# Performance work log

Hardware: AMD Instinct MI355X
Metric: run time of the kernel (lower is better)

## Reference

```python
import jax, jax.numpy as jnp
import numpy as np

STAGE = 100  # number of weight bins


def _bin_reconstruct(w, affine):
    # Faithful vectorization of the 100-iter binning loop: element in bin i
    # (half-open interval) gets scaled by affine[i]; the max element falls
    # outside every bin (w < wmin + stage*range/stage fails) and is zeroed.
    flat = w.reshape(-1)
    wmin, wmax = flat.min(), flat.max()
    idx = jnp.floor((flat - wmin) / (wmax - wmin) * STAGE).astype(jnp.int32)
    mask = (idx < STAGE).astype(flat.dtype)  # mask is detached in torch (non-diff anyway)
    scale = affine[jnp.clip(idx, 0, STAGE - 1)]
    return flat * scale * mask


def _kl_vs_laplace(new_flat, lap):
    # F.kl_div(log_softmax(w), softmax(lap), reduction='none').mean()
    logq = jax.nn.log_softmax(new_flat)
    p = jax.nn.softmax(lap)
    return (p * (jnp.log(p) - logq)).mean()


def _adder2d(x, w, stride, padding, groups=1):
    # AdderNet conv: out = -sum_k |patch_k - w_k| (no bias)
    O, Cg, kh, kw = w.shape
    patches = jax.lax.conv_general_dilated_patches(
        x, (kh, kw), (stride, stride), [(padding, padding), (padding, padding)])
    B, _, Hp, Wp = patches.shape  # channel dim ordered (C, kh, kw), C-major
    if groups == 1:
        p = patches.reshape(B, 1, Cg * kh * kw, Hp, Wp)
        wf = w.reshape(1, O, Cg * kh * kw, 1, 1)
    else:  # depthwise: groups == C_in, Cg == 1, O == C_in
        p = patches.reshape(B, O, kh * kw, Hp, Wp)
        wf = w.reshape(1, O, kh * kw, 1, 1)
    return -jnp.abs(p - wf).sum(axis=2)  # [B, O, Hp, Wp]


def _bn_train(x, g, b, eps=1e-5):
    # BatchNorm2d in training mode (batch statistics, biased variance)
    m = x.mean(axis=(0, 2, 3), keepdims=True)
    v = ((x - m) ** 2).mean(axis=(0, 2, 3), keepdims=True)
    return (x - m) * jax.lax.rsqrt(v + eps) * g.reshape(1, -1, 1, 1) + b.reshape(1, -1, 1, 1)


def _forward(x, sw_ds, sw_c1, sw_c2, sw_c3, a_ds, a_c1, a_c2, a_c3, peg_w,
             g1, b1, g2, b2, g3, b3, gds, bds, lap_ds, lap_c1, lap_c2, lap_c3):
    kl = jnp.float32(0.0)
    f_ds = _bin_reconstruct(sw_ds, a_ds)
    kl = kl + _kl_vs_laplace(f_ds, lap_ds)
    f_c1 = _bin_reconstruct(sw_c1, a_c1)
    kl = kl + _kl_vs_laplace(f_c1, lap_c1)
    residual = jax.nn.relu(_bn_train(_adder2d(x, f_ds.reshape(sw_ds.shape), 1, 0), gds, bds))
    h = _adder2d(x, f_c1.reshape(sw_c1.shape), 1, 0)
    h = _adder2d(h, peg_w, 1, 1, groups=peg_w.shape[0])  # PEG depthwise 3x3
    h = jax.nn.relu(_bn_train(h, g1, b1))
    f_c2 = _bin_reconstruct(sw_c2, a_c2)
    kl = kl + _kl_vs_laplace(f_c2, lap_c2)
    h = _adder2d(h, f_c2.reshape(sw_c2.shape), 1, 1)
    h = jax.nn.relu(_bn_train(h, g2, b2))
    f_c3 = _bin_reconstruct(sw_c3, a_c3)
    kl = kl + _kl_vs_laplace(f_c3, lap_c3)
    h = _adder2d(h, f_c3.reshape(sw_c3.shape), 1, 0)
    h = _bn_train(h, g3, b3)  # bn3 gamma zero-initialized
    return jax.nn.relu(h + residual), kl


def setup_inputs() -> dict:
    key = jax.random.key(0)
    ks = jax.random.split(key, 16)
    inp = {
        'x': jax.random.normal(ks[0], (4, 128, 28, 28), jnp.float32),
        'sw_downsample': jax.random.normal(ks[1], (256, 128, 1, 1), jnp.float32) * 0.05,
        'sw_conv1': jax.random.normal(ks[2], (64, 128, 1, 1), jnp.float32) * 0.05,
        'sw_conv2': jax.random.normal(ks[3], (64, 64, 3, 3), jnp.float32) * 0.05,
        'sw_conv3': jax.random.normal(ks[4], (256, 64, 1, 1), jnp.float32) * 0.05,
        'downsample_affine': jax.random.normal(ks[5], (100,), jnp.float32),
        'conv1_affine': jax.random.normal(ks[6], (100,), jnp.float32),
        'conv2_affine': jax.random.normal(ks[7], (100,), jnp.float32),
        'conv3_affine': jax.random.normal(ks[8], (100,), jnp.float32),
        'peg_w': jax.random.normal(ks[9], (64, 1, 3, 3), jnp.float32) * 0.05,
        'bn1_g': jnp.ones((64,), jnp.float32), 'bn1_b': jnp.zeros((64,), jnp.float32),
        'bn2_g': jnp.ones((64,), jnp.float32), 'bn2_b': jnp.zeros((64,), jnp.float32),
        'bn3_g': jnp.zeros((256,), jnp.float32), 'bn3_b': jnp.zeros((256,), jnp.float32),
        'bnds_g': jnp.ones((256,), jnp.float32), 'bnds_b': jnp.zeros((256,), jnp.float32),
        # Laplace(0, 2) samples, drawn once in setup so the reference is deterministic
        'lap_ds': jax.random.laplace(ks[10], (32768,), jnp.float32) * 2.0,
        'lap_c1': jax.random.laplace(ks[11], (8192,), jnp.float32) * 2.0,
        'lap_c2': jax.random.laplace(ks[12], (36864,), jnp.float32) * 2.0,
        'lap_c3': jax.random.laplace(ks[13], (16384,), jnp.float32) * 2.0,
    }
    return inp


def reference(x, sw_downsample, sw_conv1, sw_conv2, sw_conv3,
              downsample_affine, conv1_affine, conv2_affine, conv3_affine, peg_w,
              bn1_g, bn1_b, bn2_g, bn2_b, bn3_g, bn3_b, bnds_g, bnds_b,
              lap_ds, lap_c1, lap_c2, lap_c3):
    return _forward(x, sw_downsample, sw_conv1, sw_conv2, sw_conv3,
                    downsample_affine, conv1_affine, conv2_affine, conv3_affine, peg_w,
                    bn1_g, bn1_b, bn2_g, bn2_b, bn3_g, bn3_b, bnds_g, bnds_b,
                    lap_ds, lap_c1, lap_c2, lap_c3)
```

## Files before the change

kernel.cpp:

```cpp
#include <hip/hip_runtime.h>
#include <math.h>


#define HW 784
#define NB 4
#define STAGE 100

__device__ __forceinline__ float wredSum(float v){
  for (int o = 32; o > 0; o >>= 1) v += __shfl_down(v, o, 64);
  return v;
}
__device__ __forceinline__ float wredMax(float v){
  for (int o = 32; o > 0; o >>= 1) v = fmaxf(v, __shfl_down(v, o, 64));
  return v;
}
__device__ __forceinline__ float wredMin(float v){
  for (int o = 32; o > 0; o >>= 1) v = fminf(v, __shfl_down(v, o, 64));
  return v;
}
__device__ __forceinline__ double wredSumD(double v){
  for (int o = 32; o > 0; o >>= 1) v += __shfl_down(v, o, 64);
  return v;
}

__device__ float blockMin4(float v){
  __shared__ float shn[4];
  __syncthreads();
  v = wredMin(v);
  if ((threadIdx.x & 63) == 0) shn[threadIdx.x >> 6] = v;
  __syncthreads();
  return fminf(fminf(shn[0], shn[1]), fminf(shn[2], shn[3]));
}
__device__ float blockMax4(float v){
  __shared__ float shx[4];
  __syncthreads();
  v = wredMax(v);
  if ((threadIdx.x & 63) == 0) shx[threadIdx.x >> 6] = v;
  __syncthreads();
  return fmaxf(fmaxf(shx[0], shx[1]), fmaxf(shx[2], shx[3]));
}

__device__ void stats4(float v0, float v1, float v2, float v3,
                       double* sumP, double* sqP, int oc0){
  __shared__ double sred[4][8];
  __syncthreads();
  const int w = threadIdx.x >> 6;
  float vv[4] = {v0, v1, v2, v3};
  #pragma unroll
  for (int i = 0; i < 4; i++){
    double d = (double)vv[i];
    double s = wredSumD(d);
    double q = wredSumD(d * d);
    if ((threadIdx.x & 63) == 0){ sred[w][i] = s; sred[w][4 + i] = q; }
  }
  __syncthreads();
  if (threadIdx.x < 8){
    double tot = sred[0][threadIdx.x] + sred[1][threadIdx.x]
               + sred[2][threadIdx.x] + sred[3][threadIdx.x];
    int i = threadIdx.x & 3;
    if (threadIdx.x < 4) atomicAdd(&sumP[oc0 + i], tot);
    else                 atomicAdd(&sqP[oc0 + i],  tot);
  }
}
__device__ void stats2(float v0, float v1, double* sumP, double* sqP, int oc0){
  __shared__ double sred2[4][4];
  __syncthreads();
  const int w = threadIdx.x >> 6;
  float vv[2] = {v0, v1};
  #pragma unroll
  for (int i = 0; i < 2; i++){
    double d = (double)vv[i];
    double s = wredSumD(d);
    double q = wredSumD(d * d);
    if ((threadIdx.x & 63) == 0){ sred2[w][i] = s; sred2[w][2 + i] = q; }
  }
  __syncthreads();
  if (threadIdx.x < 4){
    double tot = sred2[0][threadIdx.x] + sred2[1][threadIdx.x]
               + sred2[2][threadIdx.x] + sred2[3][threadIdx.x];
    int i = threadIdx.x & 1;
    if (threadIdx.x < 2) atomicAdd(&sumP[oc0 + i], tot);
    else                 atomicAdd(&sqP[oc0 + i],  tot);
  }
}

__device__ void klAccum(float se, float sel, float sef, float sq, double* dst){
  __shared__ double kls[4][4];
  __syncthreads();
  const int w = threadIdx.x >> 6;
  double a0 = wredSumD((double)se);
  double a1 = wredSumD((double)sel);
  double a2 = wredSumD((double)sef);
  double a3 = wredSumD((double)sq);
  if ((threadIdx.x & 63) == 0){
    kls[w][0] = a0; kls[w][1] = a1; kls[w][2] = a2; kls[w][3] = a3;
  }
  __syncthreads();
  if (threadIdx.x < 4){
    double tot = kls[0][threadIdx.x] + kls[1][threadIdx.x]
               + kls[2][threadIdx.x] + kls[3][threadIdx.x];
    atomicAdd(&dst[threadIdx.x], tot);
  }
}

__device__ __forceinline__ float reconv(float vv, float mn, float rng,
                                        const float* saff){
  float q = (vv - mn) / rng * 100.0f;
  int idx = (int)floorf(q);
  float nv = 0.0f;
  if (idx < STAGE){
    int ci = idx < 0 ? 0 : (idx > STAGE - 1 ? STAGE - 1 : idx);
    nv = vv * saff[ci];
  }
  return nv;
}

__device__ __forceinline__ void mmReduce(const float* mmbuf, int tens,
                                         float& mn, float& mx){
  mn = 3.402823466e38f; mx = -3.402823466e38f;
  #pragma unroll
  for (int k = 0; k < 16; k++){
    mn = fminf(mn, mmbuf[tens * 32 + k]);
    mx = fmaxf(mx, mmbuf[tens * 32 + 16 + k]);
  }
}

__global__ __launch_bounds__(256) void minmax_kernel(
    const float* w0, int n0, const float* w1, int n1,
    const float* w2, int n2, const float* w3, int n3,
    float* mmbuf, double* dstat)
{
  if (threadIdx.x < 21) dstat[blockIdx.x * 21 + threadIdx.x] = 0.0;
  const int tens = blockIdx.x >> 4, slot = blockIdx.x & 15;
  const float* w; int n;
  if      (tens == 0){ w = w0; n = n0; }
  else if (tens == 1){ w = w1; n = n1; }
  else if (tens == 2){ w = w2; n = n2; }
  else               { w = w3; n = n3; }
  float mn = 3.402823466e38f, mx = -3.402823466e38f;
  for (int i = slot * 256 + threadIdx.x; i < n; i += 4096){
    float v = w[i];
    mn = fminf(mn, v); mx = fmaxf(mx, v);
  }
  mn = blockMin4(mn); mx = blockMax4(mx);
  if (threadIdx.x == 0){
    mmbuf[tens * 32 + slot]      = mn;
    mmbuf[tens * 32 + 16 + slot] = mx;
  }
}

__global__ __launch_bounds__(256) void front_kernel(
    const float* __restrict__ x,
    const float* __restrict__ w_ds, const float* __restrict__ aff_ds,
    const float* __restrict__ lap_ds,
    const float* __restrict__ w_c1, const float* __restrict__ aff_c1,
    const float* __restrict__ lap_c1,
    const float* __restrict__ w_c2, const float* __restrict__ aff_c2,
    const float* __restrict__ lap_c2, float* __restrict__ f_c2,
    const float* __restrict__ w_c3, const float* __restrict__ aff_c3,
    const float* __restrict__ lap_c3,
    const float* __restrict__ peg_w, const float* __restrict__ mmbuf,
    float* __restrict__ A, float* __restrict__ T2, double* __restrict__ dS)
{
  const int t = threadIdx.x;
  if (blockIdx.x < 512){
    const int a = blockIdx.x;
    const int chunk = a & 3, og = (a >> 2) & 31, b = a >> 7;
    const int oc0 = og * 8;
    __shared__ float saff[STAGE];
    __shared__ float sw[1024];
    if (t < STAGE) saff[t] = aff_ds[t];
    float mn, mx; mmReduce(mmbuf, 0, mn, mx);
    const float rng = mx - mn;
    __syncthreads();
    for (int k = t; k < 1024; k += 256)
      sw[k] = reconv(w_ds[oc0 * 128 + k], mn, rng, saff);
    __syncthreads();

    const int px = chunk * 196 + t;
    float v0=0,v1=0,v2=0,v3=0,v4=0,v5=0,v6=0,v7=0;
    if (t < 196){
      const float* xp = x + (size_t)b * 128 * HW + px;
      float c0=0,c1=0,c2=0,c3=0,c4=0,c5=0,c6=0,c7=0;
      #pragma unroll 4
      for (int c = 0; c < 128; c++){
        float xv = xp[(size_t)c * HW];
        c0 += fabsf(xv - sw[c]);
        c1 += fabsf(xv - sw[128 + c]);
        c2 += fabsf(xv - sw[256 + c]);
        c3 += fabsf(xv - sw[384 + c]);
        c4 += fabsf(xv - sw[512 + c]);
        c5 += fabsf(xv - sw[640 + c]);
        c6 += fabsf(xv - sw[768 + c]);
        c7 += fabsf(xv - sw[896 + c]);
      }
      v0=-c0; v1=-c1; v2=-c2; v3=-c3; v4=-c4; v5=-c5; v6=-c6; v7=-c7;
      float* op = A + ((size_t)(b * 256 + oc0)) * HW + px;
      op[0]=v0; op[HW]=v1; op[2*HW]=v2; op[3*HW]=v3;
      op[4*HW]=v4; op[5*HW]=v5; op[6*HW]=v6; op[7*HW]=v7;
    }
    stats4(v0, v1, v2, v3, dS + 0, dS + 256, oc0);
    stats4(v4, v5, v6, v7, dS + 0, dS + 256, oc0 + 4);

    if (b == 0 && chunk == 0){
      float se = 0, sel = 0, sef = 0, sq = 0;
      for (int k = t; k < 1024; k += 256){
        float l = lap_ds[oc0 * 128 + k];
        float e = expf(l);
        se += e; sel += e * l; sef += e * sw[k];
        sq += expf(sw[k]);
      }
      klAccum(se, sel, sef, sq, dS + 1280 + 0);
    }
  } else if (blockIdx.x < 768){
    const int a = blockIdx.x - 512;
    const int rc = a & 3, og = (a >> 2) & 15, b = a >> 6;
    const int oc0 = og * 4;
    __shared__ float saffc[STAGE];
    __shared__ float swc[512];
    __shared__ float swp[36];
    __shared__ float sT1[4][256];
    if (t < STAGE) saffc[t] = aff_c1[t];
    if (t >= 128 && t < 164) swp[t - 128] = peg_w[oc0 * 9 + (t - 128)];
    float mn, mx; mmReduce(mmbuf, 1, mn, mx);
    const float rng = mx - mn;
    __syncthreads();
    for (int k = t; k < 512; k += 256)
      swc[k] = reconv(w_c1[oc0 * 128 + k], mn, rng, saffc);
    __syncthreads();

    if (t < 252){
      const int rr = t / 28;
      const int col = t - rr * 28;
      const int wr = rc * 7 - 1 + rr;
      float tv0 = 0, tv1 = 0, tv2 = 0, tv3 = 0;
      if (wr >= 0 && wr < 28){
        const float* xp = x + (size_t)b * 128 * HW + wr * 28 + col;
        float c0 = 0, c1 = 0, c2 = 0, c3 = 0;
        #pragma unroll 4
        for (int c = 0; c < 128; c++){
          float xv = xp[(size_t)c * HW];
          c0 += fabsf(xv - swc[c]);
          c1 += fabsf(xv - swc[128 + c]);
          c2 += fabsf(xv - swc[256 + c]);
          c3 += fabsf(xv - swc[384 + c]);
        }
        tv0 = -c0; tv1 = -c1; tv2 = -c2; tv3 = -c3;
      }
      sT1[0][t] = tv0; sT1[1][t] = tv1; sT1[2][t] = tv2; sT1[3][t] = tv3;
    }
    __syncthreads();
    float v0 = 0, v1 = 0, v2 = 0, v3 = 0;
    if (t < 196){
      const int r = t / 28, col = t - r * 28;
      float c0 = 0, c1 = 0, c2 = 0, c3 = 0;
      #pragma unroll
      for (int ky = 0; ky < 3; ky++){
        #pragma unroll
        for (int kx = 0; kx < 3; kx++){
          int cc = col + kx - 1;
          bool ok = (cc >= 0) && (cc < 28);
          int idx = ok ? ((r + ky) * 28 + cc) : 0;
          float p0 = ok ? sT1[0][idx] : 0.0f;
          float p1 = ok ? sT1[1][idx] : 0.0f;
          float p2 = ok ? sT1[2][idx] : 0.0f;
          float p3 = ok ? sT1[3][idx] : 0.0f;
          int wk = ky * 3 + kx;
          c0 += fabsf(p0 - swp[wk]);
          c1 += fabsf(p1 - swp[9 + wk]);
          c2 += fabsf(p2 - swp[18 + wk]);
          c3 += fabsf(p3 - swp[27 + wk]);
        }
      }
      v0 = -c0; v1 = -c1; v2 = -c2; v3 = -c3;
      const int opx = (rc * 7 + r) * 28 + col;
      float* op = T2 + ((size_t)(b * 64 + oc0)) * HW + opx;
      op[0] = v0; op[HW] = v1; op[2 * HW] = v2; op[3 * HW] = v3;
    }
    stats4(v0, v1, v2, v3, dS + 512, dS + 576, oc0);

    if (b == 0 && rc == 0){
      float se = 0, sel = 0, sef = 0, sq = 0;
      for (int k = t; k < 512; k += 256){
        float l = lap_c1[oc0 * 128 + k];
        float e = expf(l);
        se += e; sel += e * l; sef += e * swc[k];
        sq += expf(swc[k]);
      }
      klAccum(se, sel, sef, sq, dS + 1280 + 4);
    }
  } else if (blockIdx.x < 832){
    const int j = blockIdx.x - 768;
    __shared__ float saff2[STAGE];
    if (t < STAGE) saff2[t] = aff_c2[t];
    float mn, mx; mmReduce(mmbuf, 2, mn, mx);
    const float rng = mx - mn;
    __syncthreads();
    float se = 0, sel = 0, sef = 0, sq = 0;
    for (int k = t; k < 576; k += 256){
      float nv = reconv(w_c2[j * 576 + k], mn, rng, saff2);
      f_c2[j * 576 + k] = nv;
      float l = lap_c2[j * 576 + k];
      float e = expf(l);
      se += e; sel += e * l; sef += e * nv; sq += expf(nv);
    }
    klAccum(se, sel, sef, sq, dS + 1280 + 8);
  } else {
    const int j = blockIdx.x - 832;
    __shared__ float saff3[STAGE];
    if (t < STAGE) saff3[t] = aff_c3[t];
    float mn, mx; mmReduce(mmbuf, 3, mn, mx);
    const float rng = mx - mn;
    __syncthreads();
    float se = 0, sel = 0, sef = 0, sq = 0;
    for (int k = t; k < 1024; k += 256){
      float nv = reconv(w_c3[j * 1024 + k], mn, rng, saff3);
      float l = lap_c3[j * 1024 + k];
      float e = expf(l);
      se += e; sel += e * l; sef += e * nv; sq += expf(nv);
    }
    klAccum(se, sel, sef, sq, dS + 1280 + 12);
  }
}

__global__ __launch_bounds__(256) void bnapply_pad_kernel(
    const float* __restrict__ T2, float* __restrict__ T2b,
    const float* __restrict__ g1, const float* __restrict__ b1,
    const double* __restrict__ dS)
{
  const int a = blockIdx.x;
  const int c = a & 63, b = a >> 6;
  __shared__ float ssc, ssb;
  if (threadIdx.x == 0){
    double s  = dS[512 + c] * (1.0 / 3136.0);
    double vr = dS[576 + c] * (1.0 / 3136.0) - s * s;
    float scale = g1[c] * rsqrtf((float)vr + 1e-5f);
    ssc = scale; ssb = b1[c] - (float)s * scale;
  }
  __syncthreads();
  const float sc_ = ssc, bi_ = ssb;
  const float* src = T2 + (size_t)a * HW;
  float* dst = T2b + (size_t)a * 960;
  for (int i = threadIdx.x; i < 960; i += 256){
    int row = i >> 5, col = i & 31;
    float v = 0.0f;
    if (row >= 1 && row <= 28 && col >= 1 && col <= 28)
      v = fmaxf(src[(row - 1) * 28 + (col - 1)] * sc_ + bi_, 0.0f);
    dst[i] = v;
  }
}

__global__ __launch_bounds__(256) void mid3x3_kernel(
    const float* __restrict__ T2b, const float* __restrict__ f_c2,
    float* __restrict__ T3, double* __restrict__ dS)
{
  const int t = threadIdx.x;
  const int a = blockIdx.x;
  const int chunk = a & 3, og = (a >> 2) & 31, b = a >> 7;
  const int oc0 = og * 2;
  const float* __restrict__ wA = f_c2 + oc0 * 576;
  const float* __restrict__ wB = wA + 576;

  float v0 = 0, v1 = 0;
  const int px = chunk * 196 + t;
  if (t < 196){
    const int y = px / 28, xc = px - y * 28;
    const float* base = T2b + (size_t)b * 64 * 960 + y * 32 + xc;
    float c0 = 0, c1 = 0;
    #pragma unroll 2
    for (int c = 0; c < 64; c++){
      const float* p = base + c * 960;
      float t0 = p[0],  t1 = p[1],  t2 = p[2];
      float t3 = p[32], t4 = p[33], t5 = p[34];
      float t6 = p[64], t7 = p[65], t8 = p[66];
      const float* wa = wA + c * 9;
      const float* wb = wB + c * 9;
      c0 += fabsf(t0 - wa[0]) + fabsf(t1 - wa[1]) + fabsf(t2 - wa[2])
          + fabsf(t3 - wa[3]) + fabsf(t4 - wa[4]) + fabsf(t5 - wa[5])
          + fabsf(t6 - wa[6]) + fabsf(t7 - wa[7]) + fabsf(t8 - wa[8]);
      c1 += fabsf(t0 - wb[0]) + fabsf(t1 - wb[1]) + fabsf(t2 - wb[2])
          + fabsf(t3 - wb[3]) + fabsf(t4 - wb[4]) + fabsf(t5 - wb[5])
          + fabsf(t6 - wb[6]) + fabsf(t7 - wb[7]) + fabsf(t8 - wb[8]);
    }
    v0 = -c0; v1 = -c1;
    T3[((size_t)(b * 64 + oc0)) * HW + px]     = v0;
    T3[((size_t)(b * 64 + oc0 + 1)) * HW + px] = v1;
  }
  stats2(v0, v1, dS + 640, dS + 704, oc0);
}

__global__ __launch_bounds__(256) void back_kernel(
    const float* __restrict__ T3, const float* __restrict__ w_c3,
    const float* __restrict__ aff_c3, const float* __restrict__ mmbuf,
    const float* __restrict__ g2, const float* __restrict__ b2,
    float* __restrict__ out, double* __restrict__ dS)
{
  const int t = threadIdx.x;
  const int a = blockIdx.x;
  const int chunk = a & 3, og = (a >> 2) & 63, b = a >> 8;
  const int oc0 = og * 4;
  __shared__ float ssc[64], ssb[64], sw[256], saff[STAGE];
  if (t < 64){
    double s  = dS[640 + t] * (1.0 / 3136.0);
    double vr = dS[704 + t] * (1.0 / 3136.0) - s * s;
    float scale = g2[t] * rsqrtf((float)vr + 1e-5f);
    ssc[t] = scale; ssb[t] = b2[t] - (float)s * scale;
  }
  if (t >= 128 && t < 128 + STAGE) saff[t - 128] = aff_c3[t - 128];
  float mn, mx; mmReduce(mmbuf, 3, mn, mx);
  const float rng = mx - mn;
  __syncthreads();
  sw[t] = reconv(w_c3[oc0 * 64 + t], mn, rng, saff);
  __syncthreads();

  const int px = chunk * 196 + t;
  float v0 = 0, v1 = 0, v2 = 0, v3 = 0;
  if (t < 196){
    const float* bp = T3 + (size_t)b * 64 * HW + px;
    float c0 = 0, c1 = 0, c2 = 0, c3 = 0;
    #pragma unroll 4
    for (int c = 0; c < 64; c++){
      float raw = bp[(size_t)c * HW];
      float vv = fmaxf(raw * ssc[c] + ssb[c], 0.0f);
      c0 += fabsf(vv - sw[c]);
      c1 += fabsf(vv - sw[64 + c]);
      c2 += fabsf(vv - sw[128 + c]);
      c3 += fabsf(vv - sw[192 + c]);
    }
    v0 = -c0; v1 = -c1; v2 = -c2; v3 = -c3;
    float* op = out + ((size_t)(b * 256 + oc0)) * HW + px;
    op[0] = v0; op[HW] = v1; op[2 * HW] = v2; op[3 * HW] = v3;
  }
  stats4(v0, v1, v2, v3, dS + 768, dS + 1024, oc0);
}

__global__ __launch_bounds__(256) void final_kernel(
    float* __restrict__ out, const float* __restrict__ A,
    const float* __restrict__ g3, const float* __restrict__ b3,
    const float* __restrict__ gds, const float* __restrict__ bds,
    const double* __restrict__ dS)
{
  __shared__ float s3c[256], s3b[256], sdc[256], sdb[256];
  const int t = threadIdx.x;
  {
    double s  = dS[768 + t] * (1.0 / 3136.0);
    double vr = dS[1024 + t] * (1.0 / 3136.0) - s * s;
    float scale = g3[t] * rsqrtf((float)vr + 1e-5f);
    s3c[t] = scale; s3b[t] = b3[t] - (float)s * scale;
    s  = dS[t] * (1.0 / 3136.0);
    vr = dS[256 + t] * (1.0 / 3136.0) - s * s;
    scale = gds[t] * rsqrtf((float)vr + 1e-5f);
    sdc[t] = scale; sdb[t] = bds[t] - (float)s * scale;
  }
  __syncthreads();
  #pragma unroll
  for (int k = 0; k < 4; k++){
    int n = blockIdx.x * 1024 + k * 256 + t;
    int c = (n / HW) & 255;
    float h = out[n], aa = A[n];
    float r = fmaxf(aa * sdc[c] + sdb[c], 0.0f);
    out[n] = fmaxf(h * s3c[c] + s3b[c] + r, 0.0f);
  }
  if (blockIdx.x == 0 && t == 0){
    const int ns[4] = {32768, 8192, 36864, 16384};
    float kl = 0.0f;
    #pragma unroll
    for (int q = 0; q < 4; q++){
      double se  = dS[1280 + q * 4];
      double sel = dS[1280 + q * 4 + 1];
      double sef = dS[1280 + q * 4 + 2];
      double sq  = dS[1280 + q * 4 + 3];
      kl += (float)((((sel - sef) / se) - log(se) + log(sq)) / (double)ns[q]);
    }
    out[802816] = kl;
  }
}

extern "C" void kernel_launch(void* const* d_in, const int* in_sizes, int n_in,
                              void* d_out, int out_size, void* d_ws, size_t ws_size,
                              hipStream_t stream)
{
  const float* x      = (const float*)d_in[0];
  const float* sw_ds  = (const float*)d_in[1];
  const float* sw_c1  = (const float*)d_in[2];
  const float* sw_c2  = (const float*)d_in[3];
  const float* sw_c3  = (const float*)d_in[4];
  const float* a_ds   = (const float*)d_in[5];
  const float* a_c1   = (const float*)d_in[6];
  const float* a_c2   = (const float*)d_in[7];
  const float* a_c3   = (const float*)d_in[8];
  const float* peg_w  = (const float*)d_in[9];
  const float* bn1_g  = (const float*)d_in[10];
  const float* bn1_b  = (const float*)d_in[11];
  const float* bn2_g  = (const float*)d_in[12];
  const float* bn2_b  = (const float*)d_in[13];
  const float* bn3_g  = (const float*)d_in[14];
  const float* bn3_b  = (const float*)d_in[15];
  const float* bnds_g = (const float*)d_in[16];
  const float* bnds_b = (const float*)d_in[17];
  const float* lap_ds = (const float*)d_in[18];
  const float* lap_c1 = (const float*)d_in[19];
  const float* lap_c2 = (const float*)d_in[20];
  const float* lap_c3 = (const float*)d_in[21];

  float* ws    = (float*)d_ws;
  float* f_c2  = ws;
  float* mmbuf = ws + 36864;
  double* dstat= (double*)(ws + 37120);
  float* A     = ws + 39808;
  float* T2    = ws + 842624;
  float* T3    = ws + 1043328;
  float* T2b   = ws + 1244032;

  float* out = (float*)d_out;

  minmax_kernel<<<64, 256, 0, stream>>>(
      sw_ds, 32768, sw_c1, 8192, sw_c2, 36864, sw_c3, 16384, mmbuf, dstat);

  front_kernel<<<848, 256, 0, stream>>>(
      x, sw_ds, a_ds, lap_ds, sw_c1, a_c1, lap_c1,
      sw_c2, a_c2, lap_c2, f_c2, sw_c3, a_c3, lap_c3,
      peg_w, mmbuf, A, T2, dstat);

  bnapply_pad_kernel<<<256, 256, 0, stream>>>(T2, T2b, bn1_g, bn1_b, dstat);

  mid3x3_kernel<<<512, 256, 0, stream>>>(T2b, f_c2, T3, dstat);

  back_kernel<<<1024, 256, 0, stream>>>(T3, sw_c3, a_c3, mmbuf,
                                        bn2_g, bn2_b, out, dstat);

  final_kernel<<<784, 256, 0, stream>>>(out, A, bn3_g, bn3_b, bnds_g, bnds_b,
                                        dstat);
}
```

Before: 171.8 us.

## Spread downsample adder conv across front, bnpad and mid kernels; transpose weights for float4 LDS

The 512 downsample-branch blocks, which have no dependency on the main path, are split across three launches: 128 in front_kernel, 192 in the BN-pad kernel and 192 in the 3x3 kernel. This fills the under-occupied BN-pad and 3x3 launches and shortens the critical front kernel. Reconstructed weights in shared memory are also transposed to channel-major so each channel's output-channel weights come from one or two float4 loads instead of several scalar LDS reads. The cost is extra shared memory and code in kernels that were previously small. The workspace offsets are also shifted.

```diff
diff --git a/kernel.cpp b/kernel.cpp
--- a/kernel.cpp
+++ b/kernel.cpp
@@ -6,10 +6,6 @@
 #define NB 4
 #define STAGE 100
 
-__device__ __forceinline__ float wredSum(float v){
-  for (int o = 32; o > 0; o >>= 1) v += __shfl_down(v, o, 64);
-  return v;
-}
 __device__ __forceinline__ float wredMax(float v){
   for (int o = 32; o > 0; o >>= 1) v = fmaxf(v, __shfl_down(v, o, 64));
   return v;
@@ -122,6 +118,65 @@
   for (int k = 0; k < 16; k++){
     mn = fminf(mn, mmbuf[tens * 32 + k]);
     mx = fmaxf(mx, mmbuf[tens * 32 + 16 + k]);
+  }
+}
+
+__device__ void dsUnit(int u, const float* __restrict__ x,
+                       const float* __restrict__ w_ds,
+                       const float* __restrict__ a_ds,
+                       const float* __restrict__ lap_ds,
+                       const float* __restrict__ mmbuf,
+                       float* __restrict__ A, double* __restrict__ dS)
+{
+  const int t = threadIdx.x;
+  const int chunk = u & 3, og = (u >> 2) & 31, b = u >> 7;
+  const int oc0 = og * 8;
+  __shared__ float saff[STAGE];
+  __shared__ float swT[1024];
+  if (t < STAGE) saff[t] = a_ds[t];
+  float mn, mx; mmReduce(mmbuf, 0, mn, mx);
+  const float rng = mx - mn;
+  __syncthreads();
+  for (int k = t; k < 1024; k += 256){
+    int loc = k >> 7, c = k & 127;
+    swT[c * 8 + loc] = reconv(w_ds[(oc0 + loc) * 128 + c], mn, rng, saff);
+  }
+  __syncthreads();
+  const float4* swT4 = (const float4*)swT;
+
+  const int px = chunk * 196 + t;
+  float v0=0,v1=0,v2=0,v3=0,v4=0,v5=0,v6=0,v7=0;
+  if (t < 196){
+    const float* xp = x + (size_t)b * 128 * HW + px;
+    float c0=0,c1=0,c2=0,c3=0,c4=0,c5=0,c6=0,c7=0;
+    #pragma unroll 4
+    for (int c = 0; c < 128; c++){
+      float xv = xp[(size_t)c * HW];
+      float4 wa = swT4[c * 2];
+      float4 wb = swT4[c * 2 + 1];
+      c0 += fabsf(xv - wa.x); c1 += fabsf(xv - wa.y);
+      c2 += fabsf(xv - wa.z); c3 += fabsf(xv - wa.w);
+      c4 += fabsf(xv - wb.x); c5 += fabsf(xv - wb.y);
+      c6 += fabsf(xv - wb.z); c7 += fabsf(xv - wb.w);
+    }
+    v0=-c0; v1=-c1; v2=-c2; v3=-c3; v4=-c4; v5=-c5; v6=-c6; v7=-c7;
+    float* op = A + ((size_t)(b * 256 + oc0)) * HW + px;
+    op[0]=v0; op[HW]=v1; op[2*HW]=v2; op[3*HW]=v3;
+    op[4*HW]=v4; op[5*HW]=v5; op[6*HW]=v6; op[7*HW]=v7;
+  }
+  stats4(v0, v1, v2, v3, dS + 0, dS + 256, oc0);
+  stats4(v4, v5, v6, v7, dS + 0, dS + 256, oc0 + 4);
+
+  if ((u & 3) == 0 && (u >> 7) == 0){
+    float se = 0, sel = 0, sef = 0, sq = 0;
+    for (int k = t; k < 1024; k += 256){
+      int loc = k >> 7, c = k & 127;
+      float f = swT[c * 8 + loc];
+      float l = lap_ds[(oc0 + loc) * 128 + c];
+      float e = expf(l);
+      se += e; sel += e * l; sef += e * f; sq += expf(f);
+    }
+    klAccum(se, sel, sef, sq, dS + 1280 + 0);
   }
 }
 
@@ -151,83 +206,37 @@
 
 __global__ __launch_bounds__(256) void front_kernel(
     const float* __restrict__ x,
-    const float* __restrict__ w_ds, const float* __restrict__ aff_ds,
+    const float* __restrict__ w_ds, const float* __restrict__ a_ds,
     const float* __restrict__ lap_ds,
-    const float* __restrict__ w_c1, const float* __restrict__ aff_c1,
+    const float* __restrict__ w_c1, const float* __restrict__ a_c1,
     const float* __restrict__ lap_c1,
-    const float* __restrict__ w_c2, const float* __restrict__ aff_c2,
+    const float* __restrict__ w_c2, const float* __restrict__ a_c2,
     const float* __restrict__ lap_c2, float* __restrict__ f_c2,
-    const float* __restrict__ w_c3, const float* __restrict__ aff_c3,
+    const float* __restrict__ w_c3, const float* __restrict__ a_c3,
     const float* __restrict__ lap_c3,
     const float* __restrict__ peg_w, const float* __restrict__ mmbuf,
     float* __restrict__ A, float* __restrict__ T2, double* __restrict__ dS)
 {
   const int t = threadIdx.x;
-  if (blockIdx.x < 512){
+  if (blockIdx.x < 256){
     const int a = blockIdx.x;
-    const int chunk = a & 3, og = (a >> 2) & 31, b = a >> 7;
-    const int oc0 = og * 8;
-    __shared__ float saff[STAGE];
-    __shared__ float sw[1024];
-    if (t < STAGE) saff[t] = aff_ds[t];
-    float mn, mx; mmReduce(mmbuf, 0, mn, mx);
-    const float rng = mx - mn;
-    __syncthreads();
-    for (int k = t; k < 1024; k += 256)
-      sw[k] = reconv(w_ds[oc0 * 128 + k], mn, rng, saff);
-    __syncthreads();
-
-    const int px = chunk * 196 + t;
-    float v0=0,v1=0,v2=0,v3=0,v4=0,v5=0,v6=0,v7=0;
-    if (t < 196){
-      const float* xp = x + (size_t)b * 128 * HW + px;
-      float c0=0,c1=0,c2=0,c3=0,c4=0,c5=0,c6=0,c7=0;
-      #pragma unroll 4
-      for (int c = 0; c < 128; c++){
-        float xv = xp[(size_t)c * HW];
-        c0 += fabsf(xv - sw[c]);
-        c1 += fabsf(xv - sw[128 + c]);
-        c2 += fabsf(xv - sw[256 + c]);
-        c3 += fabsf(xv - sw[384 + c]);
-        c4 += fabsf(xv - sw[512 + c]);
-        c5 += fabsf(xv - sw[640 + c]);
-        c6 += fabsf(xv - sw[768 + c]);
-        c7 += fabsf(xv - sw[896 + c]);
-      }
-      v0=-c0; v1=-c1; v2=-c2; v3=-c3; v4=-c4; v5=-c5; v6=-c6; v7=-c7;
-      float* op = A + ((size_t)(b * 256 + oc0)) * HW + px;
-      op[0]=v0; op[HW]=v1; op[2*HW]=v2; op[3*HW]=v3;
-      op[4*HW]=v4; op[5*HW]=v5; op[6*HW]=v6; op[7*HW]=v7;
-    }
-    stats4(v0, v1, v2, v3, dS + 0, dS + 256, oc0);
-    stats4(v4, v5, v6, v7, dS + 0, dS + 256, oc0 + 4);
-
-    if (b == 0 && chunk == 0){
-      float se = 0, sel = 0, sef = 0, sq = 0;
-      for (int k = t; k < 1024; k += 256){
-        float l = lap_ds[oc0 * 128 + k];
-        float e = expf(l);
-        se += e; sel += e * l; sef += e * sw[k];
-        sq += expf(sw[k]);
-      }
-      klAccum(se, sel, sef, sq, dS + 1280 + 0);
-    }
-  } else if (blockIdx.x < 768){
-    const int a = blockIdx.x - 512;
     const int rc = a & 3, og = (a >> 2) & 15, b = a >> 6;
     const int oc0 = og * 4;
     __shared__ float saffc[STAGE];
-    __shared__ float swc[512];
+    __shared__ float swcT[512];
     __shared__ float swp[36];
     __shared__ float sT1[4][256];
-    if (t < STAGE) saffc[t] = aff_c1[t];
+    if (t < STAGE) saffc[t] = a_c1[t];
     if (t >= 128 && t < 164) swp[t - 128] = peg_w[oc0 * 9 + (t - 128)];
     float mn, mx; mmReduce(mmbuf, 1, mn, mx);
     const float rng = mx - mn;
     __syncthreads();
-    for (int k = t; k < 512; k += 256)
-      swc[k] = reconv(w_c1[oc0 * 128 + k], mn, rng, saffc);
+    for (int k = t; k < 512; k += 256){
+      int loc = k >> 7, c = k & 127;
+      swcT[c * 4 + loc] = reconv(w_c1[(oc0 + loc) * 128 + c], mn, rng, saffc);
+    }
     __syncthreads();
+    const float4* swcT4 = (const float4*)swcT;
 
     if (t < 252){
       const int rr = t / 28;
@@ -240,10 +249,11 @@
         #pragma unroll 4
         for (int c = 0; c < 128; c++){
           float xv = xp[(size_t)c * HW];
-          c0 += fabsf(xv - swc[c]);
-          c1 += fabsf(xv - swc[128 + c]);
-          c2 += fabsf(xv - swc[256 + c]);
-          c3 += fabsf(xv - swc[384 + c]);
+          float4 wv = swcT4[c];
+          c0 += fabsf(xv - wv.x);
+          c1 += fabsf(xv - wv.y);
+          c2 += fabsf(xv - wv.z);
+          c3 += fabsf(xv - wv.w);
         }
         tv0 = -c0; tv1 = -c1; tv2 = -c2; tv3 = -c3;
       }
@@ -282,17 +292,20 @@
     if (b == 0 && rc == 0){
       float se = 0, sel = 0, sef = 0, sq = 0;
       for (int k = t; k < 512; k += 256){
-        float l = lap_c1[oc0 * 128 + k];
+        int loc = k >> 7, c = k & 127;
+        float f = swcT[c * 4 + loc];
+        float l = lap_c1[(oc0 + loc) * 128 + c];
         float e = expf(l);
-        se += e; sel += e * l; sef += e * swc[k];
-        sq += expf(swc[k]);
+        se += e; sel += e * l; sef += e * f; sq += expf(f);
       }
       klAccum(se, sel, sef, sq, dS + 1280 + 4);
     }
-  } else if (blockIdx.x < 832){
-    const int j = blockIdx.x - 768;
+  } else if (blockIdx.x < 384){
+    dsUnit(blockIdx.x - 256, x, w_ds, a_ds, lap_ds, mmbuf, A, dS);
+  } else if (blockIdx.x < 448){
+    const int j = blockIdx.x - 384;
     __shared__ float saff2[STAGE];
-    if (t < STAGE) saff2[t] = aff_c2[t];
+    if (t < STAGE) saff2[t] = a_c2[t];
     float mn, mx; mmReduce(mmbuf, 2, mn, mx);
     const float rng = mx - mn;
     __syncthreads();
@@ -306,9 +319,9 @@
     }
     klAccum(se, sel, sef, sq, dS + 1280 + 8);
   } else {
-    const int j = blockIdx.x - 832;
+    const int j = blockIdx.x - 448;
     __shared__ float saff3[STAGE];
-    if (t < STAGE) saff3[t] = aff_c3[t];
+    if (t < STAGE) saff3[t] = a_c3[t];
     float mn, mx; mmReduce(mmbuf, 3, mn, mx);
     const float rng = mx - mn;
     __syncthreads();
@@ -323,75 +336,90 @@
   }
 }
 
-__global__ __launch_bounds__(256) void bnapply_pad_kernel(
+__global__ __launch_bounds__(256) void bnpad_kernel(
     const float* __restrict__ T2, float* __restrict__ T2b,
     const float* __restrict__ g1, const float* __restrict__ b1,
-    const double* __restrict__ dS)
-{
-  const int a = blockIdx.x;
-  const int c = a & 63, b = a >> 6;
-  __shared__ float ssc, ssb;
-  if (threadIdx.x == 0){
-    double s  = dS[512 + c] * (1.0 / 3136.0);
-    double vr = dS[576 + c] * (1.0 / 3136.0) - s * s;
-    float scale = g1[c] * rsqrtf((float)vr + 1e-5f);
-    ssc = scale; ssb = b1[c] - (float)s * scale;
-  }
-  __syncthreads();
-  const float sc_ = ssc, bi_ = ssb;
-  const float* src = T2 + (size_t)a * HW;
-  float* dst = T2b + (size_t)a * 960;
-  for (int i = threadIdx.x; i < 960; i += 256){
-    int row = i >> 5, col = i & 31;
-    float v = 0.0f;
-    if (row >= 1 && row <= 28 && col >= 1 && col <= 28)
-      v = fmaxf(src[(row - 1) * 28 + (col - 1)] * sc_ + bi_, 0.0f);
-    dst[i] = v;
+    const float* __restrict__ x, const float* __restrict__ w_ds,
+    const float* __restrict__ a_ds, const float* __restrict__ lap_ds,
+    const float* __restrict__ mmbuf, float* __restrict__ A,
+    double* __restrict__ dS)
+{
+  if (blockIdx.x < 256){
+    const int a = blockIdx.x;
+    const int c = a & 63;
+    __shared__ float ssc, ssb;
+    if (threadIdx.x == 0){
+      double s  = dS[512 + c] * (1.0 / 3136.0);
+      double vr = dS[576 + c] * (1.0 / 3136.0) - s * s;
+      float scale = g1[c] * rsqrtf((float)vr + 1e-5f);
+      ssc = scale; ssb = b1[c] - (float)s * scale;
+    }
+    __syncthreads();
+    const float sc_ = ssc, bi_ = ssb;
+    const float* src = T2 + (size_t)a * HW;
+    float* dst = T2b + (size_t)a * 960;
+    for (int i = threadIdx.x; i < 960; i += 256){
+      int row = i >> 5, col = i & 31;
+      float v = 0.0f;
+      if (row >= 1 && row <= 28 && col >= 1 && col <= 28)
+        v = fmaxf(src[(row - 1) * 28 + (col - 1)] * sc_ + bi_, 0.0f);
+      dst[i] = v;
+    }
+  } else {
+    dsUnit(128 + (blockIdx.x - 256), x, w_ds, a_ds, lap_ds, mmbuf, A, dS);
   }
 }
 
 __global__ __launch_bounds__(256) void mid3x3_kernel(
     const float* __restrict__ T2b, const float* __restrict__ f_c2,
-    float* __restrict__ T3, double* __restrict__ dS)
-{
-  const int t = threadIdx.x;
-  const int a = blockIdx.x;
-  const int chunk = a & 3, og = (a >> 2) & 31, b = a >> 7;
-  const int oc0 = og * 2;
-  const float* __restrict__ wA = f_c2 + oc0 * 576;
-  const float* __restrict__ wB = wA + 576;
-
-  float v0 = 0, v1 = 0;
-  const int px = chunk * 196 + t;
-  if (t < 196){
-    const int y = px / 28, xc = px - y * 28;
-    const float* base = T2b + (size_t)b * 64 * 960 + y * 32 + xc;
-    float c0 = 0, c1 = 0;
-    #pragma unroll 2
-    for (int c = 0; c < 64; c++){
-      const float* p = base + c * 960;
-      float t0 = p[0],  t1 = p[1],  t2 = p[2];
-      float t3 = p[32], t4 = p[33], t5 = p[34];
-      float t6 = p[64], t7 = p[65], t8 = p[66];
-      const float* wa = wA + c * 9;
-      const float* wb = wB + c * 9;
-      c0 += fabsf(t0 - wa[0]) + fabsf(t1 - wa[1]) + fabsf(t2 - wa[2])
-          + fabsf(t3 - wa[3]) + fabsf(t4 - wa[4]) + fabsf(t5 - wa[5])
-          + fabsf(t6 - wa[6]) + fabsf(t7 - wa[7]) + fabsf(t8 - wa[8]);
-      c1 += fabsf(t0 - wb[0]) + fabsf(t1 - wb[1]) + fabsf(t2 - wb[2])
-          + fabsf(t3 - wb[3]) + fabsf(t4 - wb[4]) + fabsf(t5 - wb[5])
-          + fabsf(t6 - wb[6]) + fabsf(t7 - wb[7]) + fabsf(t8 - wb[8]);
-    }
-    v0 = -c0; v1 = -c1;
-    T3[((size_t)(b * 64 + oc0)) * HW + px]     = v0;
-    T3[((size_t)(b * 64 + oc0 + 1)) * HW + px] = v1;
-  }
-  stats2(v0, v1, dS + 640, dS + 704, oc0);
+    float* __restrict__ T3,
+    const float* __restrict__ x, const float* __restrict__ w_ds,
+    const float* __restrict__ a_ds, const float* __restrict__ lap_ds,
+    const float* __restrict__ mmbuf, float* __restrict__ A,
+    double* __restrict__ dS)
+{
+  if (blockIdx.x < 512){
+    const int t = threadIdx.x;
+    const int a = blockIdx.x;
+    const int chunk = a & 3, og = (a >> 2) & 31, b = a >> 7;
+    const int oc0 = og * 2;
+    const float* __restrict__ wA = f_c2 + oc0 * 576;
+    const float* __restrict__ wB = wA + 576;
+
+    float v0 = 0, v1 = 0;
+    const int px = chunk * 196 + t;
+    if (t < 196){
+      const int y = px / 28, xc = px - y * 28;
+      const float* base = T2b + (size_t)b * 64 * 960 + y * 32 + xc;
+      float c0 = 0, c1 = 0;
+      #pragma unroll 2
+      for (int c = 0; c < 64; c++){
+        const float* p = base + c * 960;
+        float t0 = p[0],  t1 = p[1],  t2 = p[2];
+        float t3 = p[32], t4 = p[33], t5 = p[34];
+        float t6 = p[64], t7 = p[65], t8 = p[66];
+        const float* wa = wA + c * 9;
+        const float* wb = wB + c * 9;
+        c0 += fabsf(t0 - wa[0]) + fabsf(t1 - wa[1]) + fabsf(t2 - wa[2])
+            + fabsf(t3 - wa[3]) + fabsf(t4 - wa[4]) + fabsf(t5 - wa[5])
+            + fabsf(t6 - wa[6]) + fabsf(t7 - wa[7]) + fabsf(t8 - wa[8]);
+        c1 += fabsf(t0 - wb[0]) + fabsf(t1 - wb[1]) + fabsf(t2 - wb[2])
+            + fabsf(t3 - wb[3]) + fabsf(t4 - wb[4]) + fabsf(t5 - wb[5])
+            + fabsf(t6 - wb[6]) + fabsf(t7 - wb[7]) + fabsf(t8 - wb[8]);
+      }
+      v0 = -c0; v1 = -c1;
+      T3[((size_t)(b * 64 + oc0)) * HW + px]     = v0;
+      T3[((size_t)(b * 64 + oc0 + 1)) * HW + px] = v1;
+    }
+    stats2(v0, v1, dS + 640, dS + 704, oc0);
+  } else {
+    dsUnit(320 + (blockIdx.x - 512), x, w_ds, a_ds, lap_ds, mmbuf, A, dS);
+  }
 }
 
 __global__ __launch_bounds__(256) void back_kernel(
     const float* __restrict__ T3, const float* __restrict__ w_c3,
-    const float* __restrict__ aff_c3, const float* __restrict__ mmbuf,
+    const float* __restrict__ a_c3, const float* __restrict__ mmbuf,
     const float* __restrict__ g2, const float* __restrict__ b2,
     float* __restrict__ out, double* __restrict__ dS)
 {
@@ -399,19 +427,23 @@
   const int a = blockIdx.x;
   const int chunk = a & 3, og = (a >> 2) & 63, b = a >> 8;
   const int oc0 = og * 4;
-  __shared__ float ssc[64], ssb[64], sw[256], saff[STAGE];
+  __shared__ float ssc[64], ssb[64], swbT[256], saff[STAGE];
   if (t < 64){
     double s  = dS[640 + t] * (1.0 / 3136.0);
     double vr = dS[704 + t] * (1.0 / 3136.0) - s * s;
     float scale = g2[t] * rsqrtf((float)vr + 1e-5f);
     ssc[t] = scale; ssb[t] = b2[t] - (float)s * scale;
   }
-  if (t >= 128 && t < 128 + STAGE) saff[t - 128] = aff_c3[t - 128];
+  if (t >= 128 && t < 128 + STAGE) saff[t - 128] = a_c3[t - 128];
   float mn, mx; mmReduce(mmbuf, 3, mn, mx);
   const float rng = mx - mn;
   __syncthreads();
-  sw[t] = reconv(w_c3[oc0 * 64 + t], mn, rng, saff);
-  __syncthreads();
+  {
+    int loc = t >> 6, c = t & 63;
+    swbT[c * 4 + loc] = reconv(w_c3[(oc0 + loc) * 64 + c], mn, rng, saff);
+  }
+  __syncthreads();
+  const float4* swbT4 = (const float4*)swbT;
 
   const int px = chunk * 196 + t;
   float v0 = 0, v1 = 0, v2 = 0, v3 = 0;
@@ -422,10 +454,11 @@
     for (int c = 0; c < 64; c++){
       float raw = bp[(size_t)c * HW];
       float vv = fmaxf(raw * ssc[c] + ssb[c], 0.0f);
-      c0 += fabsf(vv - sw[c]);
-      c1 += fabsf(vv - sw[64 + c]);
-      c2 += fabsf(vv - sw[128 + c]);
-      c3 += fabsf(vv - sw[192 + c]);
+      float4 wv = swbT4[c];
+      c0 += fabsf(vv - wv.x);
+      c1 += fabsf(vv - wv.y);
+      c2 += fabsf(vv - wv.z);
+      c3 += fabsf(vv - wv.w);
     }
     v0 = -c0; v1 = -c1; v2 = -c2; v3 = -c3;
     float* op = out + ((size_t)(b * 256 + oc0)) * HW + px;
@@ -506,25 +539,27 @@
   float* ws    = (float*)d_ws;
   float* f_c2  = ws;
   float* mmbuf = ws + 36864;
-  double* dstat= (double*)(ws + 37120);
-  float* A     = ws + 39808;
-  float* T2    = ws + 842624;
-  float* T3    = ws + 1043328;
-  float* T2b   = ws + 1244032;
+  double* dstat= (double*)(ws + 36992);
+  float* A     = ws + 39680;
+  float* T2    = ws + 842496;
+  float* T3    = ws + 1043200;
+  float* T2b   = ws + 1243904;
 
   float* out = (float*)d_out;
 
   minmax_kernel<<<64, 256, 0, stream>>>(
       sw_ds, 32768, sw_c1, 8192, sw_c2, 36864, sw_c3, 16384, mmbuf, dstat);
 
-  front_kernel<<<848, 256, 0, stream>>>(
+  front_kernel<<<464, 256, 0, stream>>>(
       x, sw_ds, a_ds, lap_ds, sw_c1, a_c1, lap_c1,
       sw_c2, a_c2, lap_c2, f_c2, sw_c3, a_c3, lap_c3,
       peg_w, mmbuf, A, T2, dstat);
 
-  bnapply_pad_kernel<<<256, 256, 0, stream>>>(T2, T2b, bn1_g, bn1_b, dstat);
-
-  mid3x3_kernel<<<512, 256, 0, stream>>>(T2b, f_c2, T3, dstat);
+  bnpad_kernel<<<448, 256, 0, stream>>>(T2, T2b, bn1_g, bn1_b,
+                                        x, sw_ds, a_ds, lap_ds, mmbuf, A, dstat);
+
+  mid3x3_kernel<<<704, 256, 0, stream>>>(T2b, f_c2, T3,
+                                         x, sw_ds, a_ds, lap_ds, mmbuf, A, dstat);
 
   back_kernel<<<1024, 256, 0, stream>>>(T3, sw_c3, a_c3, mmbuf,
                                         bn2_g, bn2_b, out, dstat);
```

New measurement: 188.1 us. 1.09x slower.
